# Performance work log

Hardware: AMD Instinct MI355X
Metric: run time of the kernel (lower is better)

Reference implementation:

```python
import jax, jax.numpy as jnp
import numpy as np
import math

DIM, DIM_QK, DIM_V = 1024, 128, 1024
NUM_BUCKETS, MAX_DISTANCE = 32, 128


def silu(x):
    return x * jax.nn.sigmoid(x)


def laplacian_attn_fn(x):
    mu = math.sqrt(0.5)
    std = math.sqrt(0.25 * math.pi)
    return (1.0 + jax.lax.erf((x - mu) / (std * math.sqrt(2.0)))) * 0.5


def rel_pos_bias(seq_len, table, scale):
    # causal T5 bucketing: n = q_pos - k_pos, clamped at 0
    q_pos = jnp.arange(seq_len)
    k_pos = jnp.arange(seq_len)
    rel_pos = k_pos[None, :] - q_pos[:, None]  # [i, j]
    n = jnp.maximum(-rel_pos, 0)
    max_exact = NUM_BUCKETS // 2
    is_small = n < max_exact
    n_safe = jnp.maximum(n, 1).astype(jnp.float32)
    val_if_large = max_exact + (
        jnp.log(n_safe / max_exact) / math.log(MAX_DISTANCE / max_exact)
        * (NUM_BUCKETS - max_exact)
    ).astype(jnp.int32)
    val_if_large = jnp.minimum(val_if_large, NUM_BUCKETS - 1)
    bucket = jnp.where(is_small, n, val_if_large)
    return table[bucket] * scale  # [i, j]


def setup_inputs() -> dict:
    key = jax.random.key(0)
    ks = jax.random.split(key, 8)
    B, S = 4, 2048
    lin_std_qk = 1.0 / math.sqrt(DIM)
    return {
        "x": jax.random.normal(ks[0], (B, S, DIM), dtype=jnp.float32),
        "wqk": jax.random.uniform(ks[1], (DIM, DIM_QK), minval=-lin_std_qk, maxval=lin_std_qk, dtype=jnp.float32),
        "bqk": jnp.zeros((DIM_QK,), dtype=jnp.float32),
        "gamma": 1.0 + 0.02 * jax.random.normal(ks[2], (2, DIM_QK), dtype=jnp.float32),
        "beta": jnp.zeros((2, DIM_QK), dtype=jnp.float32),
        "wv": jax.random.uniform(ks[3], (DIM, DIM_V), minval=-lin_std_qk, maxval=lin_std_qk, dtype=jnp.float32),
        "bv": jnp.zeros((DIM_V,), dtype=jnp.float32),
        "rel_bias": jax.random.normal(ks[4], (NUM_BUCKETS,), dtype=jnp.float32),
    }


def reference(x, wqk, bqk, gamma, beta, wv, bv, rel_bias):
    B, S, _ = x.shape
    qk = silu(x @ wqk + bqk)                       # [B, S, dqk]
    q = qk * gamma[0] + beta[0]
    k = qk * gamma[1] + beta[1]
    v = silu(x @ wv + bv)                          # [B, S, dv]
    scale = 1.0 / S                                # laplacian_attn_fn scaling
    sim = jnp.einsum('bid,bjd->bij', q, k) * scale
    sim = sim + rel_pos_bias(S, rel_bias, DIM_QK ** 0.5)[None, :, :]
    attn = laplacian_attn_fn(sim)
    causal_mask = jnp.triu(jnp.ones((S, S), dtype=bool), k=1)
    attn = jnp.where(causal_mask[None, :, :], 0.0, attn)
    return jnp.einsum('bij,bjd->bid', attn, v)
```

## Files before the change

kernel.cpp:

```cpp
#include <hip/hip_runtime.h>
#include <stdint.h>


#define B_   4
#define S_   2048
#define DIM_ 1024
#define DQK  128
#define DV   1024
#define NQV  1152

typedef __attribute__((ext_vector_type(8))) short short8;
typedef __attribute__((ext_vector_type(4))) float f32x4;

__device__ __forceinline__ uint16_t f32_to_bf16(float f) {
  uint32_t u = __float_as_uint(f);
  u += 0x7FFFu + ((u >> 16) & 1u);
  return (uint16_t)(u >> 16);
}

__device__ __forceinline__ uint32_t pack_bf16(float a, float b) {
  return (uint32_t)f32_to_bf16(a) | ((uint32_t)f32_to_bf16(b) << 16);
}

__device__ __forceinline__ float silu_f(float x) {
  return x * __builtin_amdgcn_rcpf(1.0f + __expf(-x));
}

__device__ __forceinline__ float laplacian_attn(float x) {
  float z  = (x - 0.70710678118654752f) * 0.79788456080286536f;
  float az = fabsf(z);
  float t  = __builtin_amdgcn_rcpf(fmaf(0.3275911f, az, 1.0f));
  float w  = fmaf(1.061405429f, t, -1.453152027f);
  w = fmaf(w, t, 1.421413741f);
  w = fmaf(w, t, -0.284496736f);
  w = fmaf(w, t, 0.254829592f);
  float P  = w * t;
  float E  = __expf(-z * z);
  float ea = fmaf(-P, E, 1.0f);
  float er = copysignf(ea, z);
  return fmaf(0.5f, er, 0.5f);
}

template <int MT, int NT>
__device__ __forceinline__ void wave_gemm_t(
    const uint16_t* __restrict__ A, int KBa, int rbA,
    const uint16_t* __restrict__ Bt, int KBb, int rbB,
    int nkb, f32x4 acc[MT][NT])
{
  const int lane = threadIdx.x & 63;

  const uint16_t* pa[MT];
  const uint16_t* pb[NT];
  #pragma unroll
  for (int mt = 0; mt < MT; mt++)
    pa[mt] = A + (size_t)(rbA + mt) * KBa * 512 + lane * 8;
  #pragma unroll
  for (int nt = 0; nt < NT; nt++)
    pb[nt] = Bt + (size_t)(rbB + nt) * KBb * 512 + lane * 8;

  #pragma unroll
  for (int mt = 0; mt < MT; mt++)
    #pragma unroll
    for (int nt = 0; nt < NT; nt++) {
      f32x4 z = {0.0f, 0.0f, 0.0f, 0.0f};
      acc[mt][nt] = z;
    }

  short8 fa0[MT], fb0[NT], fa1[MT], fb1[NT];

  auto loads = [&](short8 fa[MT], short8 fb[NT], int kb) {
    #pragma unroll
    for (int mt = 0; mt < MT; mt++)
      fa[mt] = *(const short8*)(pa[mt] + (size_t)kb * 512);
    #pragma unroll
    for (int nt = 0; nt < NT; nt++)
      fb[nt] = *(const short8*)(pb[nt] + (size_t)kb * 512);
  };
  auto mfmas = [&](short8 fa[MT], short8 fb[NT]) {
    #pragma unroll
    for (int mt = 0; mt < MT; mt++)
      #pragma unroll
      for (int nt = 0; nt < NT; nt++)
        acc[mt][nt] = __builtin_amdgcn_mfma_f32_16x16x32_bf16(
            fa[mt], fb[nt], acc[mt][nt], 0, 0, 0);
  };

  loads(fa0, fb0, 0);
  loads(fa1, fb1, 1);
  for (int kb = 2; kb < nkb; kb += 2) {
    mfmas(fa0, fb0);
    loads(fa0, fb0, kb);
    mfmas(fa1, fb1);
    loads(fa1, fb1, kb + 1);
  }
  mfmas(fa0, fb0);
  mfmas(fa1, fb1);
}

#define WAVE_PREAMBLE                                  \
  int lane = threadIdx.x & 63;                         \
  int wave = threadIdx.x >> 6;                         \
  int lane16 = lane & 15;                              \
  int quad = lane >> 4;                                \
  int wrow = (wave >> 1) * 64;                         \
  int wcol = (wave & 1) * 64;


__global__ __launch_bounds__(256) void k_prep_x(
    const float* __restrict__ x, uint16_t* __restrict__ xb)
{
  int t = blockIdx.x * 256 + threadIdx.x;
  int i16 = t & 15, oct = (t >> 4) & 3, kb = (t >> 6) & 31, ib = t >> 11;
  const float* src = x + (size_t)(ib * 16 + i16) * DIM_ + kb * 32 + oct * 8;
  float4 a = *(const float4*)src;
  float4 b = *(const float4*)(src + 4);
  short8 o;
  o[0] = f32_to_bf16(a.x); o[1] = f32_to_bf16(a.y);
  o[2] = f32_to_bf16(a.z); o[3] = f32_to_bf16(a.w);
  o[4] = f32_to_bf16(b.x); o[5] = f32_to_bf16(b.y);
  o[6] = f32_to_bf16(b.z); o[7] = f32_to_bf16(b.w);
  *(short8*)(xb + (size_t)t * 8) = o;
}

__global__ __launch_bounds__(256) void k_prep_w(
    const float* __restrict__ wqk, const float* __restrict__ wv,
    uint16_t* __restrict__ wT)
{
  int t = blockIdx.x * 256 + threadIdx.x;
  int n16 = t & 15, oct = (t >> 4) & 3, kb = (t >> 6) & 31, nb = t >> 11;
  int n = nb * 16 + n16;
  int k0 = kb * 32 + oct * 8;
  short8 o;
  if (n < DQK) {
    #pragma unroll
    for (int j = 0; j < 8; j++)
      o[j] = f32_to_bf16(wqk[(size_t)(k0 + j) * DQK + n]);
  } else {
    int nn = n - DQK;
    #pragma unroll
    for (int j = 0; j < 8; j++)
      o[j] = f32_to_bf16(wv[(size_t)(k0 + j) * DV + nn]);
  }
  *(short8*)(wT + (size_t)t * 8) = o;
}

__global__ __launch_bounds__(256) void k_bias(
    const float* __restrict__ rel, float* __restrict__ bias_n)
{
  int n = blockIdx.x * blockDim.x + threadIdx.x;
  if (n >= S_) return;
  int bucket;
  if (n < 16) {
    bucket = n;
  } else {
    float tt = logf((float)n * 0.0625f) / 2.0794415416798357f * 16.0f;
    int vl = 16 + (int)tt;
    bucket = vl < 31 ? vl : 31;
  }
  bias_n[n] = rel[bucket] * 11.313708498984761f;
}


__global__ __launch_bounds__(256, 3) void k_gemm_qkv(
    const uint16_t* __restrict__ xb, const uint16_t* __restrict__ wT,
    const float* __restrict__ bqk, const float* __restrict__ gamma,
    const float* __restrict__ beta, const float* __restrict__ bv,
    uint16_t* __restrict__ qb, uint16_t* __restrict__ kb,
    uint16_t* __restrict__ vT)
{
  int bx = blockIdx.x, by = blockIdx.y;
  WAVE_PREAMBLE
  f32x4 acc[4][4];

  if (bx == 0) {
    wave_gemm_t<4,4>(wT, DIM_ >> 5, (wave >> 1) * 4,
                     xb, DIM_ >> 5, by * 8 + (wave & 1) * 4,
                     DIM_ >> 5, acc);
    int ibase = by * 128 + (wave & 1) * 64;
    int cbase = (wave >> 1) * 64;
    #pragma unroll
    for (int mt = 0; mt < 4; mt++) {
      int c0 = cbase + mt * 16 + quad * 4;
      float4 bb = *(const float4*)(bqk + c0);
      float4 g0 = *(const float4*)(gamma + c0);
      float4 g1 = *(const float4*)(gamma + DQK + c0);
      float4 e0 = *(const float4*)(beta + c0);
      float4 e1 = *(const float4*)(beta + DQK + c0);
      size_t coff = (size_t)(c0 >> 5) * 512 + ((c0 >> 3) & 3) * 128 + (c0 & 7);
      #pragma unroll
      for (int nt = 0; nt < 4; nt++) {
        int i = ibase + nt * 16 + lane16;
        float s0 = silu_f(acc[mt][nt][0] + bb.x);
        float s1 = silu_f(acc[mt][nt][1] + bb.y);
        float s2 = silu_f(acc[mt][nt][2] + bb.z);
        float s3 = silu_f(acc[mt][nt][3] + bb.w);
        uint2 pq, pk;
        pq.x = pack_bf16(fmaf(s0, g0.x, e0.x), fmaf(s1, g0.y, e0.y));
        pq.y = pack_bf16(fmaf(s2, g0.z, e0.z), fmaf(s3, g0.w, e0.w));
        pk.x = pack_bf16(fmaf(s0, g1.x, e1.x), fmaf(s1, g1.y, e1.y));
        pk.y = pack_bf16(fmaf(s2, g1.z, e1.z), fmaf(s3, g1.w, e1.w));
        size_t off = (size_t)(i >> 4) * 4 * 512 + (size_t)(i & 15) * 8 + coff;
        *(uint2*)(qb + off) = pq;
        *(uint2*)(kb + off) = pk;
      }
    }
  } else {
    wave_gemm_t<4,4>(xb, DIM_ >> 5, by * 8 + (wave >> 1) * 4,
                     wT, DIM_ >> 5, bx * 8 + (wave & 1) * 4,
                     DIM_ >> 5, acc);
    int b = by >> 4;
    uint16_t* vt = vT + (size_t)b * DV * S_;
    #pragma unroll
    for (int nt = 0; nt < 4; nt++) {
      int n = (bx - 1) * 128 + wcol + nt * 16 + lane16;
      float bb = bv[n];
      #pragma unroll
      for (int mt = 0; mt < 4; mt++) {
        int j0l = (by & 15) * 128 + wrow + mt * 16 + quad * 4;
        uint16_t v0 = f32_to_bf16(silu_f(acc[mt][nt][0] + bb));
        uint16_t v1 = f32_to_bf16(silu_f(acc[mt][nt][1] + bb));
        uint16_t v2 = f32_to_bf16(silu_f(acc[mt][nt][2] + bb));
        uint16_t v3 = f32_to_bf16(silu_f(acc[mt][nt][3] + bb));
        size_t off = (size_t)((n >> 4) * 64 + (j0l >> 5)) * 512 +
                     ((j0l >> 3) & 3) * 128 + (n & 15) * 8 + (j0l & 7);
        uint2 pk;
        pk.x = (uint32_t)v0 | ((uint32_t)v1 << 16);
        pk.y = (uint32_t)v2 | ((uint32_t)v3 << 16);
        *(uint2*)(vt + off) = pk;
      }
    }
  }
}

__global__ __launch_bounds__(128, 4) void k_gemm_sim(
    const uint16_t* __restrict__ qb, const uint16_t* __restrict__ kb,
    const float* __restrict__ bias_n, uint16_t* __restrict__ attn)
{
  int b = blockIdx.x;
  int bt = blockIdx.y;
  int it = (int)((sqrtf(8.0f * (float)b + 1.0f) - 1.0f) * 0.5f);
  while ((it + 1) * (it + 2) / 2 <= b) ++it;
  while (it * (it + 1) / 2 > b) --it;
  int jt = b - it * (it + 1) / 2;

  int lane = threadIdx.x & 63;
  int wave = threadIdx.x >> 6;
  int lane16 = lane & 15;
  int quad = lane >> 4;

  f32x4 acc[4][2];
  wave_gemm_t<4,2>(kb, 4, bt * 128 + jt * 4,
                   qb, 4, bt * 128 + it * 4 + wave * 2,
                   4, acc);

  uint16_t* ab = attn + (size_t)bt * S_ * S_;
  int ibase = it * 64 + wave * 32;
  int jbase = jt * 64;
  #pragma unroll
  for (int nt = 0; nt < 2; nt++) {
    int i = ibase + nt * 16 + lane16;
    size_t irow = (size_t)(i >> 4) * 64 * 512 + (size_t)(i & 15) * 8;
    #pragma unroll
    for (int mt = 0; mt < 4; mt++) {
      int j0 = jbase + mt * 16 + quad * 4;
      float v[4];
      #pragma unroll
      for (int r = 0; r < 4; r++) {
        int j = j0 + r;
        float aval = 0.0f;
        if (j <= i) {
          float sim = acc[mt][nt][r] * (1.0f / 2048.0f) + bias_n[i - j];
          aval = laplacian_attn(sim);
        }
        v[r] = aval;
      }
      uint2 pk;
      pk.x = pack_bf16(v[0], v[1]);
      pk.y = pack_bf16(v[2], v[3]);
      size_t off = irow + (size_t)(j0 >> 5) * 512 + ((j0 >> 3) & 3) * 128 +
                   (j0 & 7);
      *(uint2*)(ab + off) = pk;
    }
  }
}

__global__ __launch_bounds__(256, 3) void k_gemm_out(
    const uint16_t* __restrict__ attn, const uint16_t* __restrict__ vT,
    float* __restrict__ out)
{
  int nx = blockIdx.x;
  int y = blockIdx.y;
  int bt = y >> 4, tt = y & 15;
  int it = (bt & 1) ? (15 - tt) : tt;
  int nkb = 4 * it + 4;
  WAVE_PREAMBLE
  f32x4 acc[4][4];
  wave_gemm_t<4,4>(attn + (size_t)bt * S_ * S_, 64, it * 8 + (wave >> 1) * 4,
                   vT + (size_t)bt * DV * S_, 64, nx * 8 + (wave & 1) * 4,
                   nkb, acc);
  #pragma unroll
  for (int mt = 0; mt < 4; mt++)
    #pragma unroll
    for (int nt = 0; nt < 4; nt++)
      #pragma unroll
      for (int r = 0; r < 4; r++) {
        int i = it * 128 + wrow + mt * 16 + quad * 4 + r;
        int n = nx * 128 + wcol + nt * 16 + lane16;
        out[((size_t)bt * S_ + i) * DV + n] = acc[mt][nt][r];
      }
}


extern "C" void kernel_launch(void* const* d_in, const int* in_sizes, int n_in,
                              void* d_out, int out_size, void* d_ws, size_t ws_size,
                              hipStream_t stream)
{
  const float* x     = (const float*)d_in[0];
  const float* wqk   = (const float*)d_in[1];
  const float* bqk   = (const float*)d_in[2];
  const float* gamma = (const float*)d_in[3];
  const float* beta  = (const float*)d_in[4];
  const float* wv    = (const float*)d_in[5];
  const float* bv    = (const float*)d_in[6];
  const float* rel   = (const float*)d_in[7];
  float* out = (float*)d_out;

  char* ws = (char*)d_ws;
  size_t off = 0;
  uint16_t* xb     = (uint16_t*)(ws + off); off += (size_t)B_ * S_ * DIM_ * 2;
  uint16_t* wT     = (uint16_t*)(ws + off); off += (size_t)NQV * DIM_ * 2;
  uint16_t* qb     = (uint16_t*)(ws + off); off += (size_t)B_ * S_ * DQK * 2;
  uint16_t* kb     = (uint16_t*)(ws + off); off += (size_t)B_ * S_ * DQK * 2;
  uint16_t* vT     = (uint16_t*)(ws + off); off += (size_t)B_ * DV * S_ * 2;
  uint16_t* attn   = (uint16_t*)(ws + off); off += (size_t)B_ * S_ * S_ * 2;
  float*    bias_n = (float*)(ws + off);    off += (size_t)S_ * 4;

  k_prep_x<<<dim3(B_ * S_ * DIM_ / 8 / 256), dim3(256), 0, stream>>>(x, xb);
  k_prep_w<<<dim3(NQV * DIM_ / 8 / 256), dim3(256), 0, stream>>>(wqk, wv, wT);
  k_bias<<<dim3(S_ / 256), dim3(256), 0, stream>>>(rel, bias_n);

  k_gemm_qkv<<<dim3(NQV / 128, B_ * S_ / 128), dim3(256), 0, stream>>>(
      xb, wT, bqk, gamma, beta, bv, qb, kb, vT);
  k_gemm_sim<<<dim3(528, B_), dim3(128), 0, stream>>>(
      qb, kb, bias_n, attn);
  k_gemm_out<<<dim3(DV / 128, B_ * S_ / 128), dim3(256), 0, stream>>>(
      attn, vT, out);
}
```

Baseline: 196.4 us.

## Deepen GEMM prefetch to four stages and reorder output GEMM schedule

Adds a depth-4 register prefetch variant of the wave GEMM and uses it in the QKV and output GEMMs, lowering the launch-bounds occupancy hint from 3 to 2 to leave room for the extra registers. The output GEMM moves to a 1D grid that schedules the longest causal row tiles first and groups batch/column tiles. It also swaps operands so each lane can write float4 vectors to the output instead of scalar stores. The aim is to hide global load latency and improve store coalescing and load balance, at the cost of lower occupancy.

Measured after the change: 190.7 us. -2.9%, faster.

```diff
diff --git a/kernel.cpp b/kernel.cpp
--- a/kernel.cpp
+++ b/kernel.cpp
@@ -41,7 +41,7 @@
   return fmaf(0.5f, er, 0.5f);
 }
 
-template <int MT, int NT>
+template <int MT, int NT, int DEPTH>
 __device__ __forceinline__ void wave_gemm_t(
     const uint16_t* __restrict__ A, int KBa, int rbA,
     const uint16_t* __restrict__ Bt, int KBb, int rbB,
@@ -85,16 +85,38 @@
             fa[mt], fb[nt], acc[mt][nt], 0, 0, 0);
   };
 
-  loads(fa0, fb0, 0);
-  loads(fa1, fb1, 1);
-  for (int kb = 2; kb < nkb; kb += 2) {
+  if constexpr (DEPTH == 2) {
+    loads(fa0, fb0, 0);
+    loads(fa1, fb1, 1);
+    for (int kb = 2; kb < nkb; kb += 2) {
+      mfmas(fa0, fb0);
+      loads(fa0, fb0, kb);
+      mfmas(fa1, fb1);
+      loads(fa1, fb1, kb + 1);
+    }
     mfmas(fa0, fb0);
-    loads(fa0, fb0, kb);
     mfmas(fa1, fb1);
-    loads(fa1, fb1, kb + 1);
-  }
-  mfmas(fa0, fb0);
-  mfmas(fa1, fb1);
+  } else {
+    short8 fa2[MT], fb2[NT], fa3[MT], fb3[NT];
+    loads(fa0, fb0, 0);
+    loads(fa1, fb1, 1);
+    loads(fa2, fb2, 2);
+    loads(fa3, fb3, 3);
+    for (int kb = 4; kb < nkb; kb += 4) {
+      mfmas(fa0, fb0);
+      loads(fa0, fb0, kb);
+      mfmas(fa1, fb1);
+      loads(fa1, fb1, kb + 1);
+      mfmas(fa2, fb2);
+      loads(fa2, fb2, kb + 2);
+      mfmas(fa3, fb3);
+      loads(fa3, fb3, kb + 3);
+    }
+    mfmas(fa0, fb0);
+    mfmas(fa1, fb1);
+    mfmas(fa2, fb2);
+    mfmas(fa3, fb3);
+  }
 }
 
 #define WAVE_PREAMBLE                                  \
@@ -161,7 +183,7 @@
 }
 
 
-__global__ __launch_bounds__(256, 3) void k_gemm_qkv(
+__global__ __launch_bounds__(256, 2) void k_gemm_qkv(
     const uint16_t* __restrict__ xb, const uint16_t* __restrict__ wT,
     const float* __restrict__ bqk, const float* __restrict__ gamma,
     const float* __restrict__ beta, const float* __restrict__ bv,
@@ -173,9 +195,9 @@
   f32x4 acc[4][4];
 
   if (bx == 0) {
-    wave_gemm_t<4,4>(wT, DIM_ >> 5, (wave >> 1) * 4,
-                     xb, DIM_ >> 5, by * 8 + (wave & 1) * 4,
-                     DIM_ >> 5, acc);
+    wave_gemm_t<4,4,4>(wT, DIM_ >> 5, (wave >> 1) * 4,
+                       xb, DIM_ >> 5, by * 8 + (wave & 1) * 4,
+                       DIM_ >> 5, acc);
     int ibase = by * 128 + (wave & 1) * 64;
     int cbase = (wave >> 1) * 64;
     #pragma unroll
@@ -205,9 +227,9 @@
       }
     }
   } else {
-    wave_gemm_t<4,4>(xb, DIM_ >> 5, by * 8 + (wave >> 1) * 4,
-                     wT, DIM_ >> 5, bx * 8 + (wave & 1) * 4,
-                     DIM_ >> 5, acc);
+    wave_gemm_t<4,4,4>(xb, DIM_ >> 5, by * 8 + (wave >> 1) * 4,
+                       wT, DIM_ >> 5, bx * 8 + (wave & 1) * 4,
+                       DIM_ >> 5, acc);
     int b = by >> 4;
     uint16_t* vt = vT + (size_t)b * DV * S_;
     #pragma unroll
@@ -249,9 +271,9 @@
   int quad = lane >> 4;
 
   f32x4 acc[4][2];
-  wave_gemm_t<4,2>(kb, 4, bt * 128 + jt * 4,
-                   qb, 4, bt * 128 + it * 4 + wave * 2,
-                   4, acc);
+  wave_gemm_t<4,2,2>(kb, 4, bt * 128 + jt * 4,
+                     qb, 4, bt * 128 + it * 4 + wave * 2,
+                     4, acc);
 
   uint16_t* ab = attn + (size_t)bt * S_ * S_;
   int ibase = it * 64 + wave * 32;
@@ -284,30 +306,31 @@
   }
 }
 
-__global__ __launch_bounds__(256, 3) void k_gemm_out(
+__global__ __launch_bounds__(256, 2) void k_gemm_out(
     const uint16_t* __restrict__ attn, const uint16_t* __restrict__ vT,
     float* __restrict__ out)
 {
-  int nx = blockIdx.x;
-  int y = blockIdx.y;
-  int bt = y >> 4, tt = y & 15;
-  int it = (bt & 1) ? (15 - tt) : tt;
+  int L = blockIdx.x;
+  int c = L & 7, m = L >> 3;
+  int g = c + 8 * (m & 3);
+  int it = 15 - (m >> 2);
+  int bt = g >> 3, nx = g & 7;
   int nkb = 4 * it + 4;
   WAVE_PREAMBLE
   f32x4 acc[4][4];
-  wave_gemm_t<4,4>(attn + (size_t)bt * S_ * S_, 64, it * 8 + (wave >> 1) * 4,
-                   vT + (size_t)bt * DV * S_, 64, nx * 8 + (wave & 1) * 4,
-                   nkb, acc);
-  #pragma unroll
-  for (int mt = 0; mt < 4; mt++)
-    #pragma unroll
-    for (int nt = 0; nt < 4; nt++)
-      #pragma unroll
-      for (int r = 0; r < 4; r++) {
-        int i = it * 128 + wrow + mt * 16 + quad * 4 + r;
-        int n = nx * 128 + wcol + nt * 16 + lane16;
-        out[((size_t)bt * S_ + i) * DV + n] = acc[mt][nt][r];
-      }
+  wave_gemm_t<4,4,4>(vT + (size_t)bt * DV * S_, 64, nx * 8 + (wave & 1) * 4,
+                     attn + (size_t)bt * S_ * S_, 64, it * 8 + (wave >> 1) * 4,
+                     nkb, acc);
+  float* ob = out + ((size_t)bt * S_ + it * 128 + wrow) * DV + nx * 128 + wcol;
+  #pragma unroll
+  for (int nt = 0; nt < 4; nt++) {
+    int i = nt * 16 + lane16;
+    #pragma unroll
+    for (int mt = 0; mt < 4; mt++) {
+      int n = mt * 16 + quad * 4;
+      *(float4*)(ob + (size_t)i * DV + n) = *(float4*)&acc[mt][nt];
+    }
+  }
 }
 
 
@@ -343,6 +366,6 @@
       xb, wT, bqk, gamma, beta, bv, qb, kb, vT);
   k_gemm_sim<<<dim3(528, B_), dim3(128), 0, stream>>>(
       qb, kb, bias_n, attn);
-  k_gemm_out<<<dim3(DV / 128, B_ * S_ / 128), dim3(256), 0, stream>>>(
+  k_gemm_out<<<dim3(512), dim3(256), 0, stream>>>(
       attn, vT, out);
 }
```
